# Kernel optimization log

Measured on AMD Instinct MI355X. Metric: run time of the kernel, lower is better.

## Reference

```python
import jax, jax.numpy as jnp
import numpy as np


def _gcn_conv(x, W, b, src, dst, norm, n_nodes):
    # PyG GCNConv: h = x @ W, then symmetric-normalized aggregation, then + b
    h = x @ W                                   # [N, F_out]
    msg = h[src] * norm[:, None]                # gather + scale, [E', F_out]
    agg = jax.ops.segment_sum(msg, dst, num_segments=n_nodes)
    return agg + b


def _norm_and_loops(edge_index, n_nodes):
    # add self-loops, compute D^{-1/2} (A+I) D^{-1/2} edge weights
    loop = jnp.arange(n_nodes, dtype=edge_index.dtype)
    src = jnp.concatenate([edge_index[0], loop])
    dst = jnp.concatenate([edge_index[1], loop])
    deg = jax.ops.segment_sum(jnp.ones_like(dst, dtype=jnp.float32), dst,
                              num_segments=n_nodes)
    dinv = jnp.where(deg > 0, jax.lax.rsqrt(deg), 0.0)
    norm = dinv[src] * dinv[dst]
    return src, dst, norm


def setup_inputs() -> dict:
    key = jax.random.key(0)
    ks = jax.random.split(key, 4)
    N, E, n_latent, n_dim = 50000, 800000, 128, 128
    hidden = 2 * n_latent
    x = jax.random.normal(ks[0], (N, n_latent), dtype=jnp.float32)
    edge_index = jax.random.randint(ks[1], (2, E), 0, N, dtype=jnp.int64)
    W1 = jax.random.normal(ks[2], (n_latent, hidden), dtype=jnp.float32) / np.sqrt(n_latent)
    b1 = jnp.zeros((hidden,), dtype=jnp.float32)
    W2 = jax.random.normal(ks[3], (hidden, n_dim), dtype=jnp.float32) / np.sqrt(hidden)
    b2 = jnp.zeros((n_dim,), dtype=jnp.float32)
    return {"x": x, "edge_index": edge_index, "W1": W1, "b1": b1,
            "W2": W2, "b2": b2}


def reference(x, edge_index, W1, b1, W2, b2):
    n_nodes = x.shape[0]
    src, dst, norm = _norm_and_loops(edge_index, n_nodes)
    z1 = jax.nn.relu(_gcn_conv(x, W1, b1, src, dst, norm, n_nodes))
    z2 = _gcn_conv(z1, W2, b2, src, dst, norm, n_nodes)
    return z2
```

## Files before the change

### kernel.cpp

```cpp
#include <hip/hip_runtime.h>


constexpr int F = 128;
constexpr int HID = 256;
constexpr int ECHUNK = 8192;

typedef __attribute__((ext_vector_type(8))) _Float16 f16x8;
typedef __attribute__((ext_vector_type(4))) _Float16 f16x4;
typedef __attribute__((ext_vector_type(4))) float f32x4;

__global__ __launch_bounds__(256) void k_prep(const int* __restrict__ dst,
                                              unsigned* __restrict__ bhist,
                                              const float* __restrict__ W1,
                                              const float* __restrict__ W2,
                                              const float* __restrict__ x,
                                              _Float16* __restrict__ w1t,
                                              _Float16* __restrict__ w2t,
                                              _Float16* __restrict__ xh,
                                              int E, int nbC, int n4) {
  __shared__ unsigned hist[256];
  int b = blockIdx.x;
  int tid = threadIdx.x;
  if (b < nbC) {
    hist[tid] = 0u;
    __syncthreads();
    int i0 = b * ECHUNK;
    int i1 = min(i0 + ECHUNK, E);
    for (int i = i0 + tid; i < i1; i += 256)
      atomicAdd(&hist[((unsigned)dst[i]) >> 8], 1u);
    __syncthreads();
    bhist[b * 256 + tid] = hist[tid];
  } else if (b < nbC + 128) {
    int idx = (b - nbC) * 256 + tid;
    int k = idx / HID, n = idx - k * HID;
    w1t[n * F + k] = (_Float16)W1[idx];
  } else if (b < nbC + 256) {
    int idx = (b - nbC - 128) * 256 + tid;
    int k = idx / F, n = idx - k * F;
    w2t[n * HID + k] = (_Float16)W2[idx];
  } else {
    int i = (b - nbC - 256) * 256 + tid;
    if (i < n4) {
      float4 v = ((const float4*)x)[i];
      f16x4 o;
      o.x = (_Float16)v.x; o.y = (_Float16)v.y;
      o.z = (_Float16)v.z; o.w = (_Float16)v.w;
      ((f16x4*)xh)[i] = o;
    }
  }
}

__global__ __launch_bounds__(256) void k_bscan(const unsigned* __restrict__ bhist,
                                               int nbC,
                                               unsigned* __restrict__ bbase,
                                               unsigned* __restrict__ bcur,
                                               int* __restrict__ rowptr,
                                               int P, int N, int E) {
  __shared__ unsigned wsum[4];
  int tid = threadIdx.x;
  unsigned v = 0u;
  for (int c = 0; c < nbC; ++c) v += bhist[c * 256 + tid];
  if (tid >= P) v = 0u;
  unsigned sv = v;
#pragma unroll
  for (int off = 1; off < 64; off <<= 1) {
    unsigned t = __shfl_up(sv, off);
    if ((tid & 63) >= off) sv += t;
  }
  int w = tid >> 6;
  if ((tid & 63) == 63) wsum[w] = sv;
  __syncthreads();
  unsigned wpre = 0;
  for (int k = 0; k < w; ++k) wpre += wsum[k];
  unsigned excl = wpre + sv - v;
  if (tid < P) {
    bbase[tid] = excl;
    bcur[tid] = excl;
  }
  if (tid == P - 1) bbase[P] = excl + v;
  if (tid == 0) rowptr[N] = E;
}

__global__ __launch_bounds__(256) void k_binscat(const int* __restrict__ src,
                                                 const int* __restrict__ dst,
                                                 const unsigned* __restrict__ bhist,
                                                 unsigned* __restrict__ bcur,
                                                 unsigned* __restrict__ packed, int E) {
  __shared__ unsigned hist[256];
  __shared__ unsigned basel[256];
  int tid = threadIdx.x;
  unsigned c = bhist[blockIdx.x * 256 + tid];
  if (c) basel[tid] = atomicAdd(&bcur[tid], c);
  hist[tid] = 0u;
  __syncthreads();
  int i0 = blockIdx.x * ECHUNK;
  int i1 = min(i0 + ECHUNK, E);
  for (int i = i0 + tid; i < i1; i += 256) {
    unsigned d = (unsigned)dst[i];
    unsigned b = d >> 8;
    unsigned pos = basel[b] + atomicAdd(&hist[b], 1u);
    packed[pos] = ((unsigned)src[i]) | ((d & 255u) << 16);
  }
}

__global__ __launch_bounds__(256) void k_bcsr(const unsigned* __restrict__ packed,
                                              const unsigned* __restrict__ bbase,
                                              float* __restrict__ dinv,
                                              int* __restrict__ rowptr,
                                              int* __restrict__ esrc, int N) {
  __shared__ unsigned hist[256];
  __shared__ unsigned rowloc[256];
  __shared__ unsigned cur[256];
  __shared__ unsigned wsum[4];
  int tid = threadIdx.x, b = blockIdx.x;
  int e0 = (int)bbase[b], e1 = (int)bbase[b + 1];
  hist[tid] = 0u;
  __syncthreads();
  for (int i = e0 + tid; i < e1; i += 256)
    atomicAdd(&hist[packed[i] >> 16], 1u);
  __syncthreads();
  unsigned v = hist[tid];
  unsigned sv = v;
#pragma unroll
  for (int off = 1; off < 64; off <<= 1) {
    unsigned t = __shfl_up(sv, off);
    if ((tid & 63) >= off) sv += t;
  }
  int w = tid >> 6;
  if ((tid & 63) == 63) wsum[w] = sv;
  __syncthreads();
  unsigned wpre = 0;
  for (int k = 0; k < w; ++k) wpre += wsum[k];
  unsigned excl = wpre + sv - v;
  int node = b * 256 + tid;
  if (node < N) {
    dinv[node] = rsqrtf((float)v + 1.0f);
    rowptr[node] = e0 + (int)excl;
  }
  rowloc[tid] = (unsigned)e0 + excl;
  cur[tid] = 0u;
  __syncthreads();
  for (int i = e0 + tid; i < e1; i += 256) {
    unsigned pk = packed[i];
    unsigned dl = pk >> 16;
    unsigned pos = rowloc[dl] + atomicAdd(&cur[dl], 1u);
    esrc[pos] = (int)(pk & 0xffffu);
  }
}

__global__ __launch_bounds__(256) void k_agg1(const int* __restrict__ rowptr,
                                              const int* __restrict__ esrc,
                                              const float* __restrict__ dinv,
                                              const _Float16* __restrict__ xh,
                                              _Float16* __restrict__ outp, int N) {
  int node = blockIdx.x * 16 + (threadIdx.x >> 4);
  int li = threadIdx.x & 15;
  int lanebase = (threadIdx.x & 63) & 48;
  if (node >= N) return;
  float di = dinv[node];
  float w0 = di * di;
  f16x8 svv = ((const f16x8*)(xh + (size_t)node * F))[li];
  float acc[8] = {};
  int beg = rowptr[node], end = rowptr[node + 1];
  for (int b = beg; b < end; b += 16) {
    int n = min(16, end - b);
    int s = 0;
    float w = 0.f;
    if (li < n) {
      s = esrc[b + li];
      w = dinv[s] * di;
    }
    int t = 0;
    for (; t + 7 < n; t += 8) {
      int ss[8];
      float wz[8];
#pragma unroll
      for (int j = 0; j < 8; ++j) {
        ss[j] = __shfl(s, lanebase + t + j);
        wz[j] = __shfl(w, lanebase + t + j);
      }
      f16x8 vv[8];
#pragma unroll
      for (int j = 0; j < 8; ++j)
        vv[j] = ((const f16x8*)(xh + (size_t)ss[j] * F))[li];
#pragma unroll
      for (int j = 0; j < 8; ++j)
#pragma unroll
        for (int k = 0; k < 8; ++k)
          acc[k] += (float)vv[j][k] * wz[j];
    }
    for (; t + 3 < n; t += 4) {
      int ss[4];
      float wz[4];
#pragma unroll
      for (int j = 0; j < 4; ++j) {
        ss[j] = __shfl(s, lanebase + t + j);
        wz[j] = __shfl(w, lanebase + t + j);
      }
      f16x8 vv[4];
#pragma unroll
      for (int j = 0; j < 4; ++j)
        vv[j] = ((const f16x8*)(xh + (size_t)ss[j] * F))[li];
#pragma unroll
      for (int j = 0; j < 4; ++j)
#pragma unroll
        for (int k = 0; k < 8; ++k)
          acc[k] += (float)vv[j][k] * wz[j];
    }
    for (; t < n; ++t) {
      int s0 = __shfl(s, lanebase + t);
      float wa = __shfl(w, lanebase + t);
      f16x8 v0 = ((const f16x8*)(xh + (size_t)s0 * F))[li];
#pragma unroll
      for (int k = 0; k < 8; ++k) acc[k] += (float)v0[k] * wa;
    }
  }
  f16x8 ov;
#pragma unroll
  for (int k = 0; k < 8; ++k) ov[k] = (_Float16)(acc[k] + (float)svv[k] * w0);
  ((f16x8*)(outp + (size_t)node * F))[li] = ov;
}

__global__ __launch_bounds__(256) void k_agg_out(const int* __restrict__ rowptr,
                                                 const int* __restrict__ esrc,
                                                 const float* __restrict__ dinv,
                                                 const _Float16* __restrict__ hb,
                                                 const float* __restrict__ bias,
                                                 float* __restrict__ outp, int N) {
  int node = blockIdx.x * 16 + (threadIdx.x >> 4);
  int li = threadIdx.x & 15;
  int lanebase = (threadIdx.x & 63) & 48;
  if (node >= N) return;
  float di = dinv[node];
  float w0 = di * di;
  f16x8 svv = ((const f16x8*)(hb + (size_t)node * F))[li];
  float acc[8] = {};
  int beg = rowptr[node], end = rowptr[node + 1];
  for (int b = beg; b < end; b += 16) {
    int n = min(16, end - b);
    int s = 0;
    float w = 0.f;
    if (li < n) {
      s = esrc[b + li];
      w = dinv[s] * di;
    }
    int t = 0;
    for (; t + 7 < n; t += 8) {
      int ss[8];
      float wz[8];
#pragma unroll
      for (int j = 0; j < 8; ++j) {
        ss[j] = __shfl(s, lanebase + t + j);
        wz[j] = __shfl(w, lanebase + t + j);
      }
      f16x8 vv[8];
#pragma unroll
      for (int j = 0; j < 8; ++j)
        vv[j] = ((const f16x8*)(hb + (size_t)ss[j] * F))[li];
#pragma unroll
      for (int j = 0; j < 8; ++j)
#pragma unroll
        for (int k = 0; k < 8; ++k)
          acc[k] += (float)vv[j][k] * wz[j];
    }
    for (; t + 3 < n; t += 4) {
      int ss[4];
      float wz[4];
#pragma unroll
      for (int j = 0; j < 4; ++j) {
        ss[j] = __shfl(s, lanebase + t + j);
        wz[j] = __shfl(w, lanebase + t + j);
      }
      f16x8 vv[4];
#pragma unroll
      for (int j = 0; j < 4; ++j)
        vv[j] = ((const f16x8*)(hb + (size_t)ss[j] * F))[li];
#pragma unroll
      for (int j = 0; j < 4; ++j)
#pragma unroll
        for (int k = 0; k < 8; ++k)
          acc[k] += (float)vv[j][k] * wz[j];
    }
    for (; t < n; ++t) {
      int s0 = __shfl(s, lanebase + t);
      float wa = __shfl(w, lanebase + t);
      f16x8 v0 = ((const f16x8*)(hb + (size_t)s0 * F))[li];
#pragma unroll
      for (int k = 0; k < 8; ++k) acc[k] += (float)v0[k] * wa;
    }
  }
  float4 bb0 = ((const float4*)bias)[li * 2];
  float4 bb1 = ((const float4*)bias)[li * 2 + 1];
  float4 o0, o1;
  o0.x = acc[0] + (float)svv[0] * w0 + bb0.x;
  o0.y = acc[1] + (float)svv[1] * w0 + bb0.y;
  o0.z = acc[2] + (float)svv[2] * w0 + bb0.z;
  o0.w = acc[3] + (float)svv[3] * w0 + bb0.w;
  o1.x = acc[4] + (float)svv[4] * w0 + bb1.x;
  o1.y = acc[5] + (float)svv[5] * w0 + bb1.y;
  o1.z = acc[6] + (float)svv[6] * w0 + bb1.z;
  o1.w = acc[7] + (float)svv[7] * w0 + bb1.w;
  float* orow = outp + (size_t)node * F + li * 8;
  *(float4*)orow = o0;
  *(float4*)(orow + 4) = o1;
}

__global__ __launch_bounds__(256) void k_fgemm(const _Float16* __restrict__ A,
                                               const _Float16* __restrict__ B1,
                                               const float* __restrict__ bias,
                                               const _Float16* __restrict__ B2,
                                               _Float16* __restrict__ H2, int M) {
  __shared__ _Float16 AL[64 * 128];
  __shared__ _Float16 ZL[64 * 256];
  int tid = threadIdx.x;
  int lane = tid & 63, wid = tid >> 6;
  int row0 = blockIdx.x * 64;

#pragma unroll
  for (int i = 0; i < 4; ++i) {
    int g = i * 256 + tid;
    int r = g >> 4, gi = g & 15;
    int o = r * 128 + ((gi ^ (r & 7)) * 8);
    size_t go = (size_t)(row0 + r) * 128 + gi * 8;
    *(f16x8*)&AL[o] = *(const f16x8*)&A[go];
  }
  __syncthreads();

  f32x4 acc[4][4] = {};
#pragma unroll
  for (int ks = 0; ks < 4; ++ks) {
    f16x8 ah[4], bh[4];
#pragma unroll
    for (int mf = 0; mf < 4; ++mf) {
      int r = mf * 16 + (lane & 15);
      int g = ks * 4 + (lane >> 4);
      ah[mf] = *(const f16x8*)&AL[r * 128 + ((g ^ (r & 7)) * 8)];
    }
#pragma unroll
    for (int nf = 0; nf < 4; ++nf) {
      int c = wid * 64 + nf * 16 + (lane & 15);
      bh[nf] = *(const f16x8*)&B1[(size_t)c * 128 + ks * 32 + (lane >> 4) * 8];
    }
#pragma unroll
    for (int mf = 0; mf < 4; ++mf)
#pragma unroll
      for (int nf = 0; nf < 4; ++nf)
        acc[mf][nf] = __builtin_amdgcn_mfma_f32_16x16x32_f16(
            ah[mf], bh[nf], acc[mf][nf], 0, 0, 0);
  }

#pragma unroll
  for (int mf = 0; mf < 4; ++mf) {
    int r0l = mf * 16 + (lane >> 4) * 4;
#pragma unroll
    for (int nf = 0; nf < 4; ++nf) {
      int c = wid * 64 + nf * 16 + (lane & 15);
      float bv = bias[c];
      int gi = c >> 3, ci = c & 7;
#pragma unroll
      for (int r = 0; r < 4; ++r) {
        int rr = r0l + r;
        float v = fmaxf(acc[mf][nf][r] + bv, 0.f);
        ZL[rr * 256 + ((gi ^ (rr & 7)) * 8) + ci] = (_Float16)v;
      }
    }
  }
  __syncthreads();

  f32x4 acc2[4][2] = {};
#pragma unroll
  for (int ks = 0; ks < 8; ++ks) {
    f16x8 ah[4], bh[2];
#pragma unroll
    for (int mf = 0; mf < 4; ++mf) {
      int r = mf * 16 + (lane & 15);
      int g = ks * 4 + (lane >> 4);
      ah[mf] = *(const f16x8*)&ZL[r * 256 + ((g ^ (r & 7)) * 8)];
    }
#pragma unroll
    for (int nf = 0; nf < 2; ++nf) {
      int c = wid * 32 + nf * 16 + (lane & 15);
      bh[nf] = *(const f16x8*)&B2[(size_t)c * 256 + ks * 32 + (lane >> 4) * 8];
    }
#pragma unroll
    for (int mf = 0; mf < 4; ++mf)
#pragma unroll
      for (int nf = 0; nf < 2; ++nf)
        acc2[mf][nf] = __builtin_amdgcn_mfma_f32_16x16x32_f16(
            ah[mf], bh[nf], acc2[mf][nf], 0, 0, 0);
  }

#pragma unroll
  for (int mf = 0; mf < 4; ++mf) {
    int r0 = row0 + mf * 16 + (lane >> 4) * 4;
#pragma unroll
    for (int nf = 0; nf < 2; ++nf) {
      int c = wid * 32 + nf * 16 + (lane & 15);
#pragma unroll
      for (int r = 0; r < 4; ++r)
        H2[(size_t)(r0 + r) * F + c] = (_Float16)acc2[mf][nf][r];
    }
  }
}

extern "C" void kernel_launch(void* const* d_in, const int* in_sizes, int n_in,
                              void* d_out, int out_size, void* d_ws, size_t ws_size,
                              hipStream_t stream) {
  const float* x = (const float*)d_in[0];
  const int* ei = (const int*)d_in[1];
  const float* W1 = (const float*)d_in[2];
  const float* b1 = (const float*)d_in[3];
  const float* W2 = (const float*)d_in[4];
  const float* b2 = (const float*)d_in[5];
  float* out = (float*)d_out;

  int N = in_sizes[0] / F;
  int E = in_sizes[1] / 2;
  const int* src = ei;
  const int* dst = ei + E;
  int P = (N + 255) / 256;
  int nbC = (E + ECHUNK - 1) / ECHUNK;

  char* ws = (char*)d_ws;
  size_t off = 0;
  auto allocB = [&](size_t bytes) {
    void* p = ws + off;
    off += ((bytes + 255) & ~(size_t)255);
    return p;
  };
  float* dinv = (float*)allocB((size_t)N * 4);
  int* rowptr = (int*)allocB(((size_t)N + 1) * 4);
  unsigned* bbase = (unsigned*)allocB(257 * 4);
  unsigned* bcur = (unsigned*)allocB(256 * 4);
  unsigned* bhist = (unsigned*)allocB((size_t)nbC * 256 * 4);
  unsigned* packed = (unsigned*)allocB((size_t)E * 4);
  int* esrc = (int*)allocB((size_t)E * 4);
  _Float16* xh = (_Float16*)allocB((size_t)N * F * 2);
  _Float16* agg = (_Float16*)allocB((size_t)(N + 64) * F * 2);
  _Float16* w1t = (_Float16*)allocB((size_t)F * HID * 2);
  _Float16* w2t = (_Float16*)allocB((size_t)HID * F * 2);
  _Float16* h2 = agg;

  int n4 = N * F / 4;
  int nbPrep = nbC + 256 + (n4 + 255) / 256;

  k_prep<<<nbPrep, 256, 0, stream>>>(dst, bhist, W1, W2, x, w1t, w2t, xh,
                                     E, nbC, n4);
  k_bscan<<<1, 256, 0, stream>>>(bhist, nbC, bbase, bcur, rowptr, P, N, E);
  k_binscat<<<nbC, 256, 0, stream>>>(src, dst, bhist, bcur, packed, E);
  k_bcsr<<<P, 256, 0, stream>>>(packed, bbase, dinv, rowptr, esrc, N);

  int nbAgg = (N + 15) / 16;
  int mb = (N + 63) / 64;

  k_agg1<<<nbAgg, 256, 0, stream>>>(rowptr, esrc, dinv, xh, agg, N);
  k_fgemm<<<mb, 256, 0, stream>>>(agg, w1t, b1, w2t, h2, N);
  k_agg_out<<<nbAgg, 256, 0, stream>>>(rowptr, esrc, dinv, h2, b2, out, N);
}
```

Measured before the change: 160.4 us.

## Fuse layer-1 aggregation into the two-GEMM kernel via shared memory

Merges the first-layer neighbor aggregation kernel with the fused GEMM kernel. Each 64-row block now gathers its aggregated rows straight into swizzled LDS, then runs both MFMA GEMMs. This removes a kernel launch and the global write and read of the intermediate aggregate, and reuses one LDS buffer for both stages. In exchange, each thread group handles four nodes one after another, so the gather phase has less parallelism per block, and the shared buffer needs extra barriers.

Result: slower. 169.3 us (+5.5%).

```diff
diff --git a/kernel.cpp b/kernel.cpp
--- a/kernel.cpp
+++ b/kernel.cpp
@@ -148,77 +148,170 @@
   }
 }
 
-__global__ __launch_bounds__(256) void k_agg1(const int* __restrict__ rowptr,
-                                              const int* __restrict__ esrc,
-                                              const float* __restrict__ dinv,
-                                              const _Float16* __restrict__ xh,
-                                              _Float16* __restrict__ outp, int N) {
-  int node = blockIdx.x * 16 + (threadIdx.x >> 4);
-  int li = threadIdx.x & 15;
-  int lanebase = (threadIdx.x & 63) & 48;
-  if (node >= N) return;
-  float di = dinv[node];
-  float w0 = di * di;
-  f16x8 svv = ((const f16x8*)(xh + (size_t)node * F))[li];
-  float acc[8] = {};
-  int beg = rowptr[node], end = rowptr[node + 1];
-  for (int b = beg; b < end; b += 16) {
-    int n = min(16, end - b);
-    int s = 0;
-    float w = 0.f;
-    if (li < n) {
-      s = esrc[b + li];
-      w = dinv[s] * di;
-    }
-    int t = 0;
-    for (; t + 7 < n; t += 8) {
-      int ss[8];
-      float wz[8];
-#pragma unroll
-      for (int j = 0; j < 8; ++j) {
-        ss[j] = __shfl(s, lanebase + t + j);
-        wz[j] = __shfl(w, lanebase + t + j);
+__global__ __launch_bounds__(256) void k_l1(const int* __restrict__ rowptr,
+                                            const int* __restrict__ esrc,
+                                            const float* __restrict__ dinv,
+                                            const _Float16* __restrict__ xh,
+                                            const _Float16* __restrict__ B1,
+                                            const float* __restrict__ bias,
+                                            const _Float16* __restrict__ B2,
+                                            _Float16* __restrict__ H2, int N) {
+  __shared__ _Float16 SL[64 * 256];
+  _Float16* AL = SL;
+  int tid = threadIdx.x;
+  int lane = tid & 63, wid = tid >> 6;
+  int row0 = blockIdx.x * 64;
+  int li = tid & 15;
+  int grp = tid >> 4;
+  int lanebase = lane & 48;
+
+  for (int it = 0; it < 4; ++it) {
+    int r = grp * 4 + it;
+    int node = row0 + r;
+    f16x8 ov = {};
+    if (node < N) {
+      float di = dinv[node];
+      float w0 = di * di;
+      f16x8 svv = ((const f16x8*)(xh + (size_t)node * F))[li];
+      float acc[8] = {};
+      int beg = rowptr[node], end = rowptr[node + 1];
+      for (int b = beg; b < end; b += 16) {
+        int n = min(16, end - b);
+        int s = 0;
+        float w = 0.f;
+        if (li < n) {
+          s = esrc[b + li];
+          w = dinv[s] * di;
+        }
+        int t = 0;
+        for (; t + 7 < n; t += 8) {
+          int ss[8];
+          float wz[8];
+#pragma unroll
+          for (int j = 0; j < 8; ++j) {
+            ss[j] = __shfl(s, lanebase + t + j);
+            wz[j] = __shfl(w, lanebase + t + j);
+          }
+          f16x8 vv[8];
+#pragma unroll
+          for (int j = 0; j < 8; ++j)
+            vv[j] = ((const f16x8*)(xh + (size_t)ss[j] * F))[li];
+#pragma unroll
+          for (int j = 0; j < 8; ++j)
+#pragma unroll
+            for (int k = 0; k < 8; ++k)
+              acc[k] += (float)vv[j][k] * wz[j];
+        }
+        for (; t + 3 < n; t += 4) {
+          int ss[4];
+          float wz[4];
+#pragma unroll
+          for (int j = 0; j < 4; ++j) {
+            ss[j] = __shfl(s, lanebase + t + j);
+            wz[j] = __shfl(w, lanebase + t + j);
+          }
+          f16x8 vv[4];
+#pragma unroll
+          for (int j = 0; j < 4; ++j)
+            vv[j] = ((const f16x8*)(xh + (size_t)ss[j] * F))[li];
+#pragma unroll
+          for (int j = 0; j < 4; ++j)
+#pragma unroll
+            for (int k = 0; k < 8; ++k)
+              acc[k] += (float)vv[j][k] * wz[j];
+        }
+        for (; t < n; ++t) {
+          int s0 = __shfl(s, lanebase + t);
+          float wa = __shfl(w, lanebase + t);
+          f16x8 v0 = ((const f16x8*)(xh + (size_t)s0 * F))[li];
+#pragma unroll
+          for (int k = 0; k < 8; ++k) acc[k] += (float)v0[k] * wa;
+        }
       }
-      f16x8 vv[8];
-#pragma unroll
-      for (int j = 0; j < 8; ++j)
-        vv[j] = ((const f16x8*)(xh + (size_t)ss[j] * F))[li];
-#pragma unroll
-      for (int j = 0; j < 8; ++j)
-#pragma unroll
-        for (int k = 0; k < 8; ++k)
-          acc[k] += (float)vv[j][k] * wz[j];
-    }
-    for (; t + 3 < n; t += 4) {
-      int ss[4];
-      float wz[4];
-#pragma unroll
-      for (int j = 0; j < 4; ++j) {
-        ss[j] = __shfl(s, lanebase + t + j);
-        wz[j] = __shfl(w, lanebase + t + j);
+#pragma unroll
+      for (int k = 0; k < 8; ++k)
+        ov[k] = (_Float16)(acc[k] + (float)svv[k] * w0);
+    }
+    *(f16x8*)&AL[r * 128 + ((li ^ (r & 7)) * 8)] = ov;
+  }
+  __syncthreads();
+
+  f32x4 acc1[4][4] = {};
+#pragma unroll
+  for (int ks = 0; ks < 4; ++ks) {
+    f16x8 ah[4], bh[4];
+#pragma unroll
+    for (int mf = 0; mf < 4; ++mf) {
+      int r = mf * 16 + (lane & 15);
+      int g = ks * 4 + (lane >> 4);
+      ah[mf] = *(const f16x8*)&AL[r * 128 + ((g ^ (r & 7)) * 8)];
+    }
+#pragma unroll
+    for (int nf = 0; nf < 4; ++nf) {
+      int c = wid * 64 + nf * 16 + (lane & 15);
+      bh[nf] = *(const f16x8*)&B1[(size_t)c * 128 + ks * 32 + (lane >> 4) * 8];
+    }
+#pragma unroll
+    for (int mf = 0; mf < 4; ++mf)
+#pragma unroll
+      for (int nf = 0; nf < 4; ++nf)
+        acc1[mf][nf] = __builtin_amdgcn_mfma_f32_16x16x32_f16(
+            ah[mf], bh[nf], acc1[mf][nf], 0, 0, 0);
+  }
+  __syncthreads();
+
+#pragma unroll
+  for (int mf = 0; mf < 4; ++mf) {
+    int r0l = mf * 16 + (lane >> 4) * 4;
+#pragma unroll
+    for (int nf = 0; nf < 4; ++nf) {
+      int c = wid * 64 + nf * 16 + (lane & 15);
+      float bv = bias[c];
+      int gi = c >> 3, ci = c & 7;
+#pragma unroll
+      for (int r = 0; r < 4; ++r) {
+        int rr = r0l + r;
+        float v = fmaxf(acc1[mf][nf][r] + bv, 0.f);
+        SL[rr * 256 + ((gi ^ (rr & 7)) * 8) + ci] = (_Float16)v;
       }
-      f16x8 vv[4];
-#pragma unroll
-      for (int j = 0; j < 4; ++j)
-        vv[j] = ((const f16x8*)(xh + (size_t)ss[j] * F))[li];
-#pragma unroll
-      for (int j = 0; j < 4; ++j)
-#pragma unroll
-        for (int k = 0; k < 8; ++k)
-          acc[k] += (float)vv[j][k] * wz[j];
-    }
-    for (; t < n; ++t) {
-      int s0 = __shfl(s, lanebase + t);
-      float wa = __shfl(w, lanebase + t);
-      f16x8 v0 = ((const f16x8*)(xh + (size_t)s0 * F))[li];
-#pragma unroll
-      for (int k = 0; k < 8; ++k) acc[k] += (float)v0[k] * wa;
-    }
-  }
-  f16x8 ov;
-#pragma unroll
-  for (int k = 0; k < 8; ++k) ov[k] = (_Float16)(acc[k] + (float)svv[k] * w0);
-  ((f16x8*)(outp + (size_t)node * F))[li] = ov;
+    }
+  }
+  __syncthreads();
+
+  f32x4 acc2[4][2] = {};
+#pragma unroll
+  for (int ks = 0; ks < 8; ++ks) {
+    f16x8 ah[4], bh[2];
+#pragma unroll
+    for (int mf = 0; mf < 4; ++mf) {
+      int r = mf * 16 + (lane & 15);
+      int g = ks * 4 + (lane >> 4);
+      ah[mf] = *(const f16x8*)&SL[r * 256 + ((g ^ (r & 7)) * 8)];
+    }
+#pragma unroll
+    for (int nf = 0; nf < 2; ++nf) {
+      int c = wid * 32 + nf * 16 + (lane & 15);
+      bh[nf] = *(const f16x8*)&B2[(size_t)c * 256 + ks * 32 + (lane >> 4) * 8];
+    }
+#pragma unroll
+    for (int mf = 0; mf < 4; ++mf)
+#pragma unroll
+      for (int nf = 0; nf < 2; ++nf)
+        acc2[mf][nf] = __builtin_amdgcn_mfma_f32_16x16x32_f16(
+            ah[mf], bh[nf], acc2[mf][nf], 0, 0, 0);
+  }
+
+#pragma unroll
+  for (int mf = 0; mf < 4; ++mf) {
+    int r0 = row0 + mf * 16 + (lane >> 4) * 4;
+#pragma unroll
+    for (int nf = 0; nf < 2; ++nf) {
+      int c = wid * 32 + nf * 16 + (lane & 15);
+#pragma unroll
+      for (int r = 0; r < 4; ++r)
+        H2[(size_t)(r0 + r) * F + c] = (_Float16)acc2[mf][nf][r];
+    }
+  }
 }
 
 __global__ __launch_bounds__(256) void k_agg_out(const int* __restrict__ rowptr,
@@ -305,104 +398,6 @@
   *(float4*)(orow + 4) = o1;
 }
 
-__global__ __launch_bounds__(256) void k_fgemm(const _Float16* __restrict__ A,
-                                               const _Float16* __restrict__ B1,
-                                               const float* __restrict__ bias,
-                                               const _Float16* __restrict__ B2,
-                                               _Float16* __restrict__ H2, int M) {
-  __shared__ _Float16 AL[64 * 128];
-  __shared__ _Float16 ZL[64 * 256];
-  int tid = threadIdx.x;
-  int lane = tid & 63, wid = tid >> 6;
-  int row0 = blockIdx.x * 64;
-
-#pragma unroll
-  for (int i = 0; i < 4; ++i) {
-    int g = i * 256 + tid;
-    int r = g >> 4, gi = g & 15;
-    int o = r * 128 + ((gi ^ (r & 7)) * 8);
-    size_t go = (size_t)(row0 + r) * 128 + gi * 8;
-    *(f16x8*)&AL[o] = *(const f16x8*)&A[go];
-  }
-  __syncthreads();
-
-  f32x4 acc[4][4] = {};
-#pragma unroll
-  for (int ks = 0; ks < 4; ++ks) {
-    f16x8 ah[4], bh[4];
-#pragma unroll
-    for (int mf = 0; mf < 4; ++mf) {
-      int r = mf * 16 + (lane & 15);
-      int g = ks * 4 + (lane >> 4);
-      ah[mf] = *(const f16x8*)&AL[r * 128 + ((g ^ (r & 7)) * 8)];
-    }
-#pragma unroll
-    for (int nf = 0; nf < 4; ++nf) {
-      int c = wid * 64 + nf * 16 + (lane & 15);
-      bh[nf] = *(const f16x8*)&B1[(size_t)c * 128 + ks * 32 + (lane >> 4) * 8];
-    }
-#pragma unroll
-    for (int mf = 0; mf < 4; ++mf)
-#pragma unroll
-      for (int nf = 0; nf < 4; ++nf)
-        acc[mf][nf] = __builtin_amdgcn_mfma_f32_16x16x32_f16(
-            ah[mf], bh[nf], acc[mf][nf], 0, 0, 0);
-  }
-
-#pragma unroll
-  for (int mf = 0; mf < 4; ++mf) {
-    int r0l = mf * 16 + (lane >> 4) * 4;
-#pragma unroll
-    for (int nf = 0; nf < 4; ++nf) {
-      int c = wid * 64 + nf * 16 + (lane & 15);
-      float bv = bias[c];
-      int gi = c >> 3, ci = c & 7;
-#pragma unroll
-      for (int r = 0; r < 4; ++r) {
-        int rr = r0l + r;
-        float v = fmaxf(acc[mf][nf][r] + bv, 0.f);
-        ZL[rr * 256 + ((gi ^ (rr & 7)) * 8) + ci] = (_Float16)v;
-      }
-    }
-  }
-  __syncthreads();
-
-  f32x4 acc2[4][2] = {};
-#pragma unroll
-  for (int ks = 0; ks < 8; ++ks) {
-    f16x8 ah[4], bh[2];
-#pragma unroll
-    for (int mf = 0; mf < 4; ++mf) {
-      int r = mf * 16 + (lane & 15);
-      int g = ks * 4 + (lane >> 4);
-      ah[mf] = *(const f16x8*)&ZL[r * 256 + ((g ^ (r & 7)) * 8)];
-    }
-#pragma unroll
-    for (int nf = 0; nf < 2; ++nf) {
-      int c = wid * 32 + nf * 16 + (lane & 15);
-      bh[nf] = *(const f16x8*)&B2[(size_t)c * 256 + ks * 32 + (lane >> 4) * 8];
-    }
-#pragma unroll
-    for (int mf = 0; mf < 4; ++mf)
-#pragma unroll
-      for (int nf = 0; nf < 2; ++nf)
-        acc2[mf][nf] = __builtin_amdgcn_mfma_f32_16x16x32_f16(
-            ah[mf], bh[nf], acc2[mf][nf], 0, 0, 0);
-  }
-
-#pragma unroll
-  for (int mf = 0; mf < 4; ++mf) {
-    int r0 = row0 + mf * 16 + (lane >> 4) * 4;
-#pragma unroll
-    for (int nf = 0; nf < 2; ++nf) {
-      int c = wid * 32 + nf * 16 + (lane & 15);
-#pragma unroll
-      for (int r = 0; r < 4; ++r)
-        H2[(size_t)(r0 + r) * F + c] = (_Float16)acc2[mf][nf][r];
-    }
-  }
-}
-
 extern "C" void kernel_launch(void* const* d_in, const int* in_sizes, int n_in,
                               void* d_out, int out_size, void* d_ws, size_t ws_size,
                               hipStream_t stream) {
@@ -436,10 +431,9 @@
   unsigned* packed = (unsigned*)allocB((size_t)E * 4);
   int* esrc = (int*)allocB((size_t)E * 4);
   _Float16* xh = (_Float16*)allocB((size_t)N * F * 2);
-  _Float16* agg = (_Float16*)allocB((size_t)(N + 64) * F * 2);
+  _Float16* h2 = (_Float16*)allocB((size_t)(N + 64) * F * 2);
   _Float16* w1t = (_Float16*)allocB((size_t)F * HID * 2);
   _Float16* w2t = (_Float16*)allocB((size_t)HID * F * 2);
-  _Float16* h2 = agg;
 
   int n4 = N * F / 4;
   int nbPrep = nbC + 256 + (n4 + 255) / 256;
@@ -450,10 +444,9 @@
   k_binscat<<<nbC, 256, 0, stream>>>(src, dst, bhist, bcur, packed, E);
   k_bcsr<<<P, 256, 0, stream>>>(packed, bbase, dinv, rowptr, esrc, N);
 
+  int mb = (N + 63) / 64;
   int nbAgg = (N + 15) / 16;
-  int mb = (N + 63) / 64;
-
-  k_agg1<<<nbAgg, 256, 0, stream>>>(rowptr, esrc, dinv, xh, agg, N);
-  k_fgemm<<<mb, 256, 0, stream>>>(agg, w1t, b1, w2t, h2, N);
+
+  k_l1<<<mb, 256, 0, stream>>>(rowptr, esrc, dinv, xh, w1t, b1, w2t, h2, N);
   k_agg_out<<<nbAgg, 256, 0, stream>>>(rowptr, esrc, dinv, h2, b2, out, N);
 }
```
